# Kernel tuning notes

Hardware: AMD Instinct MI355X
Metric: run time of the kernel (lower is better)

## Reference

```python
import math
import jax, jax.numpy as jnp
import numpy as np

N_HEADS = 8

def setup_inputs() -> dict:
    key = jax.random.key(0)
    bs, n_heads, ch, l = 4, N_HEADS, 64, 1024
    width = 3 * n_heads * ch      # 1536 (packed q,k,v channels)
    T = 3 * l                     # 3072 (three spatial bands: ll, lh, hl)
    qkv = jax.random.normal(key, (bs, width, T), dtype=jnp.float32)
    return {"qkv": qkv, "l": l}

def reference(qkv, l):
    n_heads = N_HEADS
    bs, width, T = qkv.shape
    ch = width // (3 * n_heads)
    q, k, v = jnp.split(qkv, 3, axis=1)              # each (bs, n_heads*ch, T)
    scale = 1.0 / math.sqrt(math.sqrt(ch))
    qh = (q * scale).reshape(bs * n_heads, ch, T)
    kh = (k * scale).reshape(bs * n_heads, ch, T)
    vh = v.reshape(bs * n_heads, ch, T)
    # The original computes attention separately for q[:, :, :l], [l:2l], [2l:],
    # but k/v (and the softmax axis s) are identical, so computing attention
    # over the full query once and splitting the output is the same math.
    attn = jnp.einsum('bct,bcs->bts', qh, kh)        # (bs*H, T, T)
    w = jax.nn.softmax(attn.astype(jnp.float32), axis=-1).astype(attn.dtype)
    agg = jnp.einsum('bts,bcs->bct', w, vh).reshape(bs, n_heads * ch, T)
    return (agg[:, :, :l], agg[:, :, l:2 * l], agg[:, :, 2 * l:])
```

## Files before the change

### kernel.cpp

```cpp
#include <hip/hip_runtime.h>
#include <hip/hip_bf16.h>
#include <stdint.h>

#define T      3072
#define CH     64
#define HEADS  32
#define BM     128
#define BN     64
#define NIT    (T / BN)

typedef unsigned short u16;
typedef short short8 __attribute__((ext_vector_type(8)));
typedef float floatx4 __attribute__((ext_vector_type(4)));

__device__ __forceinline__ unsigned pk2(float a, float b) {
  union { __hip_bfloat162 h; unsigned u; } cv;
  cv.h = __float22bfloat162_rn(float2{a, b});
  return cv.u;
}

__device__ __forceinline__ void gl_lds16(const void* g, void* l) {
  __builtin_amdgcn_global_load_lds(
      (const __attribute__((address_space(1))) uint32_t*)g,
      (__attribute__((address_space(3))) uint32_t*)l, 16, 0, 0);
}

__device__ __forceinline__ void pl32swap(unsigned& x, unsigned& y) {
#if __has_builtin(__builtin_amdgcn_permlane32_swap)
  auto r = __builtin_amdgcn_permlane32_swap(x, y, false, false);
  x = r[0]; y = r[1];
#else
  asm("v_permlane32_swap_b32 %0, %1" : "+v"(x), "+v"(y));
#endif
}
__device__ __forceinline__ void pl16swap(unsigned& x, unsigned& y) {
#if __has_builtin(__builtin_amdgcn_permlane16_swap)
  auto r = __builtin_amdgcn_permlane16_swap(x, y, false, false);
  x = r[0]; y = r[1];
#else
  asm("v_permlane16_swap_b32 %0, %1" : "+v"(x), "+v"(y));
#endif
}

__global__ __launch_bounds__(256) void qktrans(
    const float* __restrict__ qkv, u16* __restrict__ Qt, u16* __restrict__ Kt,
    u16* __restrict__ Vo) {
  __shared__ __align__(16) u16 tl[64][72];
  const int ttile = blockIdx.x, hh = blockIdx.y, role = blockIdx.z;
  const int b = hh >> 3, h = hh & 7;
  const int t0 = ttile * 64;
  const int tid = threadIdx.x;

  if (role == 2) {
    const float* vsrc = qkv + (size_t)(b * 1536 + 1024 + h * CH) * T;
    u16* vdst = Vo + (size_t)(b * 512 + h * CH) * T;
#pragma unroll
    for (int p = 0; p < 2; ++p) {
      const int r = p * 32 + (tid >> 3);
      const int off = (tid & 7) * 8;
      const float4* s4 = (const float4*)(vsrc + (size_t)r * T + t0 + off);
      float4 a = s4[0], c = s4[1];
      uint4 o;
      o.x = pk2(a.x, a.y); o.y = pk2(a.z, a.w);
      o.z = pk2(c.x, c.y); o.w = pk2(c.z, c.w);
      *(uint4*)(vdst + (size_t)r * T + t0 + off) = o;
    }
    return;
  }

  const float* src = qkv + (size_t)(b * 1536 + role * 512 + h * CH) * T;
  const float scale = (role == 0) ? 0.18033688011112042f : 1.0f;

#pragma unroll
  for (int p = 0; p < 2; ++p) {
    const int c0 = p * 32 + ((tid >> 4) << 1);
    const int ts = (tid & 15) * 4;
    float4 a = *(const float4*)(src + (size_t)c0 * T + t0 + ts);
    float4 c = *(const float4*)(src + (size_t)(c0 + 1) * T + t0 + ts);
    *(unsigned*)&tl[ts + 0][c0] = pk2(a.x * scale, c.x * scale);
    *(unsigned*)&tl[ts + 1][c0] = pk2(a.y * scale, c.y * scale);
    *(unsigned*)&tl[ts + 2][c0] = pk2(a.z * scale, c.z * scale);
    *(unsigned*)&tl[ts + 3][c0] = pk2(a.w * scale, c.w * scale);
  }
  __syncthreads();
  u16* dst = (role == 0 ? Qt : Kt) + (size_t)hh * T * CH;
#pragma unroll
  for (int q = 0; q < 2; ++q) {
    const int t = q * 32 + (tid >> 3);
    const int cc = (tid & 7) * 8;
    uint4 v = *(const uint4*)&tl[t][cc];
    *(uint4*)(dst + (size_t)(t0 + t) * CH + cc) = v;
  }
}

__global__ __launch_bounds__(256, 3) void attn(
    const u16* __restrict__ Qt, const u16* __restrict__ Kt,
    const u16* __restrict__ Vg, float* __restrict__ out) {
  __shared__ __align__(16) u16 KB[2][BN * CH];
  __shared__ __align__(16) u16 VB[2][CH * BN];

  const int qtile = blockIdx.x, hh = blockIdx.y;
  const int tid = threadIdx.x;
  const int wave = tid >> 6, lane = tid & 63;
  const int l15 = lane & 15, quad = lane >> 4;
  const int t0 = qtile * BM + wave * 32;

  const u16* Qh = Qt + (size_t)hh * T * CH;
  const u16* Kh = Kt + (size_t)hh * T * CH;
  const u16* Vh = Vg + (size_t)hh * CH * T;

  short8 qf[2][2];
#pragma unroll
  for (int tq = 0; tq < 2; ++tq)
#pragma unroll
    for (int kc = 0; kc < 2; ++kc)
      qf[tq][kc] = *(const short8*)(Qh + (size_t)(t0 + tq * 16 + l15) * CH + kc * 32 + quad * 8);

  floatx4 oacc[2][4] = {};
  float lsum[2][2] = {};

  int srow[2], scb[2];
#pragma unroll
  for (int j = 0; j < 2; ++j) {
    const int p = wave * 128 + j * 64 + lane;
    srow[j] = p >> 3;
    scb[j]  = (p & 7) ^ ((srow[j] + 2 * (srow[j] >> 3)) & 7);
  }
  const int swl = (l15 + 2 * (l15 >> 3)) & 7;

#define STAGE(buf, s0)                                                              \
  do {                                                                              \
    _Pragma("unroll")                                                               \
    for (int j = 0; j < 2; ++j)                                                     \
      gl_lds16(Kh + (size_t)((s0) + srow[j]) * CH + scb[j] * 8,                     \
               &KB[buf][(wave * 128 + j * 64) * 8]);                                \
    _Pragma("unroll")                                                               \
    for (int j = 0; j < 2; ++j)                                                     \
      gl_lds16(Vh + (size_t)srow[j] * T + (s0) + scb[j] * 8,                        \
               &VB[buf][(wave * 128 + j * 64) * 8]);                                \
  } while (0)

  STAGE(0, 0);

  for (int it = 0; it < NIT; ++it) {
    const int cur = it & 1;
    __syncthreads();
    if (it + 1 < NIT) STAGE(cur ^ 1, (it + 1) * BN);

    const u16* KL = KB[cur];
    const u16* VL = VB[cur];

    floatx4 sacc[2][4];
#pragma unroll
    for (int nt = 0; nt < 4; ++nt) {
      const int ph0 = quad ^ swl ^ ((nt & 1) * 4);
      const int base = (nt * 16 + l15) * CH;
      const short8 kf0 = *(const short8*)(KL + base + ph0 * 8);
      const short8 kf1 = *(const short8*)(KL + base + (ph0 ^ 4) * 8);
#pragma unroll
      for (int tq = 0; tq < 2; ++tq) {
        floatx4 z = {0.f, 0.f, 0.f, 0.f};
        z = __builtin_amdgcn_mfma_f32_16x16x32_bf16(kf0, qf[tq][0], z, 0, 0, 0);
        z = __builtin_amdgcn_mfma_f32_16x16x32_bf16(kf1, qf[tq][1], z, 0, 0, 0);
        sacc[tq][nt] = z;
      }
    }

    unsigned Apk[2][4], Bpk[2][4];
#pragma unroll
    for (int tq = 0; tq < 2; ++tq)
#pragma unroll
      for (int nt = 0; nt < 4; ++nt) {
        floatx4 sv = sacc[tq][nt];
        float p0 = __builtin_amdgcn_exp2f(sv[0]);
        float p1 = __builtin_amdgcn_exp2f(sv[1]);
        float p2 = __builtin_amdgcn_exp2f(sv[2]);
        float p3 = __builtin_amdgcn_exp2f(sv[3]);
        lsum[tq][nt & 1] += (p0 + p1) + (p2 + p3);
        Apk[tq][nt] = pk2(p0, p1);
        Bpk[tq][nt] = pk2(p2, p3);
      }

#pragma unroll
    for (int ks = 0; ks < 2; ++ks) {
      short8 pf[2];
#pragma unroll
      for (int tq = 0; tq < 2; ++tq) {
        unsigned a0 = Apk[tq][2 * ks], a1 = Apk[tq][2 * ks + 1];
        unsigned b0 = Bpk[tq][2 * ks], b1 = Bpk[tq][2 * ks + 1];
        pl32swap(a0, a1); pl16swap(a0, a1);
        pl32swap(b0, b1); pl16swap(b0, b1);
        union { uint4 u; short8 s; } pw;
        pw.u.x = a0; pw.u.y = b0; pw.u.z = a1; pw.u.w = b1;
        pf[tq] = pw.s;
      }
#pragma unroll
      for (int mt = 0; mt < 4; ++mt) {
        const int ph = quad ^ swl ^ ((mt & 1) * 4) ^ (ks * 4);
        const short8 vf = *(const short8*)(VL + (mt * 16 + l15) * BN + ph * 8);
        oacc[0][mt] = __builtin_amdgcn_mfma_f32_16x16x32_bf16(pf[0], vf, oacc[0][mt], 0, 0, 0);
        oacc[1][mt] = __builtin_amdgcn_mfma_f32_16x16x32_bf16(pf[1], vf, oacc[1][mt], 0, 0, 0);
      }
    }
  }

  float ls[2];
#pragma unroll
  for (int tq = 0; tq < 2; ++tq) {
    float s = lsum[tq][0] + lsum[tq][1];
    s += __shfl_xor(s, 16, 64);
    s += __shfl_xor(s, 32, 64);
    ls[tq] = s;
  }
  float linv[2][4];
#pragma unroll
  for (int tq = 0; tq < 2; ++tq)
#pragma unroll
    for (int r = 0; r < 4; ++r)
      linv[tq][r] = 1.0f / __shfl(ls[tq], quad * 4 + r, 64);

  const int b = hh >> 3, h = hh & 7;
#pragma unroll
  for (int tq = 0; tq < 2; ++tq) {
    const int tg = t0 + tq * 16 + quad * 4;
    const int band = tg >> 10, tt = tg & 1023;
    float* obase = out + (size_t)band * (4 * 512 * 1024)
                       + (size_t)b * (512 * 1024)
                       + (size_t)(h * CH) * 1024 + tt;
#pragma unroll
    for (int mt = 0; mt < 4; ++mt) {
      const int c = mt * 16 + l15;
      float4 v;
      v.x = oacc[tq][mt][0] * linv[tq][0];
      v.y = oacc[tq][mt][1] * linv[tq][1];
      v.z = oacc[tq][mt][2] * linv[tq][2];
      v.w = oacc[tq][mt][3] * linv[tq][3];
      *(float4*)(obase + (size_t)c * 1024) = v;
    }
  }
}

extern "C" void kernel_launch(void* const* d_in, const int* in_sizes, int n_in,
                              void* d_out, int out_size, void* d_ws, size_t ws_size,
                              hipStream_t stream) {
  (void)in_sizes; (void)n_in; (void)out_size; (void)ws_size;
  const float* qkv = (const float*)d_in[0];
  u16* Qt = (u16*)d_ws;
  u16* Kt = Qt + (size_t)HEADS * T * CH;
  u16* Vo = Kt + (size_t)HEADS * T * CH;
  float* out = (float*)d_out;

  qktrans<<<dim3(T / 64, HEADS, 3), 256, 0, stream>>>(qkv, Qt, Kt, Vo);
  attn<<<dim3(T / BM, HEADS), 256, 0, stream>>>(Qt, Kt, Vo, out);
}
```

Baseline: 218.5 us.

## Split query tile across 8 waves and compute row sums via MFMA

The attention block now uses 512 threads (8 waves), each owning 16 query rows instead of 32. This halves per-wave register state and doubles wave-level parallelism. The per-row softmax denominator is now accumulated by an extra MFMA against a ones vector, replacing the VALU adds and cross-lane shuffles. In exchange, each K/V tile loaded into LDS is reused across fewer MFMAs per wave, and the rowsum is computed from bf16-rounded probabilities.

```diff
diff --git a/kernel.cpp b/kernel.cpp
--- a/kernel.cpp
+++ b/kernel.cpp
@@ -93,7 +93,7 @@
   }
 }
 
-__global__ __launch_bounds__(256, 3) void attn(
+__global__ __launch_bounds__(512, 6) void attn(
     const u16* __restrict__ Qt, const u16* __restrict__ Kt,
     const u16* __restrict__ Vg, float* __restrict__ out) {
   __shared__ __align__(16) u16 KB[2][BN * CH];
@@ -103,41 +103,33 @@
   const int tid = threadIdx.x;
   const int wave = tid >> 6, lane = tid & 63;
   const int l15 = lane & 15, quad = lane >> 4;
-  const int t0 = qtile * BM + wave * 32;
+  const int t0 = qtile * BM + wave * 16;
 
   const u16* Qh = Qt + (size_t)hh * T * CH;
   const u16* Kh = Kt + (size_t)hh * T * CH;
   const u16* Vh = Vg + (size_t)hh * CH * T;
 
-  short8 qf[2][2];
-#pragma unroll
-  for (int tq = 0; tq < 2; ++tq)
-#pragma unroll
-    for (int kc = 0; kc < 2; ++kc)
-      qf[tq][kc] = *(const short8*)(Qh + (size_t)(t0 + tq * 16 + l15) * CH + kc * 32 + quad * 8);
-
-  floatx4 oacc[2][4] = {};
-  float lsum[2][2] = {};
-
-  int srow[2], scb[2];
-#pragma unroll
-  for (int j = 0; j < 2; ++j) {
-    const int p = wave * 128 + j * 64 + lane;
-    srow[j] = p >> 3;
-    scb[j]  = (p & 7) ^ ((srow[j] + 2 * (srow[j] >> 3)) & 7);
-  }
+  short8 qf[2];
+#pragma unroll
+  for (int kc = 0; kc < 2; ++kc)
+    qf[kc] = *(const short8*)(Qh + (size_t)(t0 + l15) * CH + kc * 32 + quad * 8);
+
+  short8 ones = {0x3F80, 0x3F80, 0x3F80, 0x3F80, 0x3F80, 0x3F80, 0x3F80, 0x3F80};
+
+  floatx4 oacc[4] = {};
+  floatx4 lacc = {0.f, 0.f, 0.f, 0.f};
+
+  const int p = wave * 64 + lane;
+  const int srow = p >> 3;
+  const int scb = (p & 7) ^ ((srow + 2 * (srow >> 3)) & 7);
   const int swl = (l15 + 2 * (l15 >> 3)) & 7;
 
 #define STAGE(buf, s0)                                                              \
   do {                                                                              \
-    _Pragma("unroll")                                                               \
-    for (int j = 0; j < 2; ++j)                                                     \
-      gl_lds16(Kh + (size_t)((s0) + srow[j]) * CH + scb[j] * 8,                     \
-               &KB[buf][(wave * 128 + j * 64) * 8]);                                \
-    _Pragma("unroll")                                                               \
-    for (int j = 0; j < 2; ++j)                                                     \
-      gl_lds16(Vh + (size_t)srow[j] * T + (s0) + scb[j] * 8,                        \
-               &VB[buf][(wave * 128 + j * 64) * 8]);                                \
+    gl_lds16(Kh + (size_t)((s0) + srow) * CH + scb * 8,                             \
+             &KB[buf][(wave * 64) * 8]);                                            \
+    gl_lds16(Vh + (size_t)srow * T + (s0) + scb * 8,                                \
+             &VB[buf][(wave * 64) * 8]);                                            \
   } while (0)
 
   STAGE(0, 0);
@@ -150,93 +142,69 @@
     const u16* KL = KB[cur];
     const u16* VL = VB[cur];
 
-    floatx4 sacc[2][4];
+    floatx4 sacc[4];
 #pragma unroll
     for (int nt = 0; nt < 4; ++nt) {
       const int ph0 = quad ^ swl ^ ((nt & 1) * 4);
       const int base = (nt * 16 + l15) * CH;
       const short8 kf0 = *(const short8*)(KL + base + ph0 * 8);
       const short8 kf1 = *(const short8*)(KL + base + (ph0 ^ 4) * 8);
-#pragma unroll
-      for (int tq = 0; tq < 2; ++tq) {
-        floatx4 z = {0.f, 0.f, 0.f, 0.f};
-        z = __builtin_amdgcn_mfma_f32_16x16x32_bf16(kf0, qf[tq][0], z, 0, 0, 0);
-        z = __builtin_amdgcn_mfma_f32_16x16x32_bf16(kf1, qf[tq][1], z, 0, 0, 0);
-        sacc[tq][nt] = z;
-      }
-    }
-
-    unsigned Apk[2][4], Bpk[2][4];
-#pragma unroll
-    for (int tq = 0; tq < 2; ++tq)
-#pragma unroll
-      for (int nt = 0; nt < 4; ++nt) {
-        floatx4 sv = sacc[tq][nt];
-        float p0 = __builtin_amdgcn_exp2f(sv[0]);
-        float p1 = __builtin_amdgcn_exp2f(sv[1]);
-        float p2 = __builtin_amdgcn_exp2f(sv[2]);
-        float p3 = __builtin_amdgcn_exp2f(sv[3]);
-        lsum[tq][nt & 1] += (p0 + p1) + (p2 + p3);
-        Apk[tq][nt] = pk2(p0, p1);
-        Bpk[tq][nt] = pk2(p2, p3);
-      }
+      floatx4 z = {0.f, 0.f, 0.f, 0.f};
+      z = __builtin_amdgcn_mfma_f32_16x16x32_bf16(kf0, qf[0], z, 0, 0, 0);
+      z = __builtin_amdgcn_mfma_f32_16x16x32_bf16(kf1, qf[1], z, 0, 0, 0);
+      sacc[nt] = z;
+    }
+
+    unsigned Apk[4], Bpk[4];
+#pragma unroll
+    for (int nt = 0; nt < 4; ++nt) {
+      floatx4 sv = sacc[nt];
+      float p0 = __builtin_amdgcn_exp2f(sv[0]);
+      float p1 = __builtin_amdgcn_exp2f(sv[1]);
+      float p2 = __builtin_amdgcn_exp2f(sv[2]);
+      float p3 = __builtin_amdgcn_exp2f(sv[3]);
+      Apk[nt] = pk2(p0, p1);
+      Bpk[nt] = pk2(p2, p3);
+    }
 
 #pragma unroll
     for (int ks = 0; ks < 2; ++ks) {
-      short8 pf[2];
-#pragma unroll
-      for (int tq = 0; tq < 2; ++tq) {
-        unsigned a0 = Apk[tq][2 * ks], a1 = Apk[tq][2 * ks + 1];
-        unsigned b0 = Bpk[tq][2 * ks], b1 = Bpk[tq][2 * ks + 1];
-        pl32swap(a0, a1); pl16swap(a0, a1);
-        pl32swap(b0, b1); pl16swap(b0, b1);
-        union { uint4 u; short8 s; } pw;
-        pw.u.x = a0; pw.u.y = b0; pw.u.z = a1; pw.u.w = b1;
-        pf[tq] = pw.s;
-      }
+      unsigned a0 = Apk[2 * ks], a1 = Apk[2 * ks + 1];
+      unsigned b0 = Bpk[2 * ks], b1 = Bpk[2 * ks + 1];
+      pl32swap(a0, a1); pl16swap(a0, a1);
+      pl32swap(b0, b1); pl16swap(b0, b1);
+      union { uint4 u; short8 s; } pw;
+      pw.u.x = a0; pw.u.y = b0; pw.u.z = a1; pw.u.w = b1;
+      const short8 pf = pw.s;
+      lacc = __builtin_amdgcn_mfma_f32_16x16x32_bf16(pf, ones, lacc, 0, 0, 0);
 #pragma unroll
       for (int mt = 0; mt < 4; ++mt) {
         const int ph = quad ^ swl ^ ((mt & 1) * 4) ^ (ks * 4);
         const short8 vf = *(const short8*)(VL + (mt * 16 + l15) * BN + ph * 8);
-        oacc[0][mt] = __builtin_amdgcn_mfma_f32_16x16x32_bf16(pf[0], vf, oacc[0][mt], 0, 0, 0);
-        oacc[1][mt] = __builtin_amdgcn_mfma_f32_16x16x32_bf16(pf[1], vf, oacc[1][mt], 0, 0, 0);
+        oacc[mt] = __builtin_amdgcn_mfma_f32_16x16x32_bf16(pf, vf, oacc[mt], 0, 0, 0);
       }
     }
   }
 
-  float ls[2];
-#pragma unroll
-  for (int tq = 0; tq < 2; ++tq) {
-    float s = lsum[tq][0] + lsum[tq][1];
-    s += __shfl_xor(s, 16, 64);
-    s += __shfl_xor(s, 32, 64);
-    ls[tq] = s;
-  }
-  float linv[2][4];
-#pragma unroll
-  for (int tq = 0; tq < 2; ++tq)
-#pragma unroll
-    for (int r = 0; r < 4; ++r)
-      linv[tq][r] = 1.0f / __shfl(ls[tq], quad * 4 + r, 64);
+  float linv[4];
+#pragma unroll
+  for (int r = 0; r < 4; ++r) linv[r] = 1.0f / lacc[r];
 
   const int b = hh >> 3, h = hh & 7;
-#pragma unroll
-  for (int tq = 0; tq < 2; ++tq) {
-    const int tg = t0 + tq * 16 + quad * 4;
-    const int band = tg >> 10, tt = tg & 1023;
-    float* obase = out + (size_t)band * (4 * 512 * 1024)
-                       + (size_t)b * (512 * 1024)
-                       + (size_t)(h * CH) * 1024 + tt;
-#pragma unroll
-    for (int mt = 0; mt < 4; ++mt) {
-      const int c = mt * 16 + l15;
-      float4 v;
-      v.x = oacc[tq][mt][0] * linv[tq][0];
-      v.y = oacc[tq][mt][1] * linv[tq][1];
-      v.z = oacc[tq][mt][2] * linv[tq][2];
-      v.w = oacc[tq][mt][3] * linv[tq][3];
-      *(float4*)(obase + (size_t)c * 1024) = v;
-    }
+  const int tg = t0 + quad * 4;
+  const int band = tg >> 10, tt = tg & 1023;
+  float* obase = out + (size_t)band * (4 * 512 * 1024)
+                     + (size_t)b * (512 * 1024)
+                     + (size_t)(h * CH) * 1024 + tt;
+#pragma unroll
+  for (int mt = 0; mt < 4; ++mt) {
+    const int c = mt * 16 + l15;
+    float4 v;
+    v.x = oacc[mt][0] * linv[0];
+    v.y = oacc[mt][1] * linv[1];
+    v.z = oacc[mt][2] * linv[2];
+    v.w = oacc[mt][3] * linv[3];
+    *(float4*)(obase + (size_t)c * 1024) = v;
   }
 }
 
@@ -251,5 +219,5 @@
   float* out = (float*)d_out;
 
   qktrans<<<dim3(T / 64, HEADS, 3), 256, 0, stream>>>(qkv, Qt, Kt, Vo);
-  attn<<<dim3(T / BM, HEADS), 256, 0, stream>>>(Qt, Kt, Vo, out);
-}
+  attn<<<dim3(T / BM, HEADS), 512, 0, stream>>>(Qt, Kt, Vo, out);
+}
```

Result: no change. 214.3 us (-1.9%).

## Split KV range across two wave groups, fuse Q conversion into attention

Applied to the files above, without the earlier changes.

The attention kernel now runs 512 threads, with two wave groups that each process half of every pair of 64-key blocks. Their partial outputs and row sums are combined through LDS at the end. Q is read directly from the fp32 input, scaled and converted inside the attention kernel, so the prep pass now handles only K and V. Row sums are computed with an MFMA against a ones vector instead of scalar adds, and V staging is restructured with an extra barrier per iteration. The aim is more parallelism per tile and one less global round trip for Q, at the cost of more barriers, the cross-group reduction, and strided uncoalesced Q loads.

```diff
diff --git a/kernel.cpp b/kernel.cpp
--- a/kernel.cpp
+++ b/kernel.cpp
@@ -7,7 +7,7 @@
 #define HEADS  32
 #define BM     128
 #define BN     64
-#define NIT    (T / BN)
+#define NIT2   (T / (2 * BN))
 
 typedef unsigned short u16;
 typedef short short8 __attribute__((ext_vector_type(8)));
@@ -42,16 +42,14 @@
 #endif
 }
 
-__global__ __launch_bounds__(256) void qktrans(
-    const float* __restrict__ qkv, u16* __restrict__ Qt, u16* __restrict__ Kt,
-    u16* __restrict__ Vo) {
-  __shared__ __align__(16) u16 tl[64][72];
+__global__ __launch_bounds__(256) void prep(
+    const float* __restrict__ qkv, u16* __restrict__ Kt, u16* __restrict__ Vo) {
   const int ttile = blockIdx.x, hh = blockIdx.y, role = blockIdx.z;
   const int b = hh >> 3, h = hh & 7;
   const int t0 = ttile * 64;
   const int tid = threadIdx.x;
 
-  if (role == 2) {
+  if (role == 1) {
     const float* vsrc = qkv + (size_t)(b * 1536 + 1024 + h * CH) * T;
     u16* vdst = Vo + (size_t)(b * 512 + h * CH) * T;
 #pragma unroll
@@ -68,22 +66,22 @@
     return;
   }
 
-  const float* src = qkv + (size_t)(b * 1536 + role * 512 + h * CH) * T;
-  const float scale = (role == 0) ? 0.18033688011112042f : 1.0f;
-
+  __shared__ __align__(16) u16 tl[64][72];
+  const float* src = qkv + (size_t)(b * 1536 + 512 + h * CH) * T;
+  const int tb = tid & 15;
 #pragma unroll
   for (int p = 0; p < 2; ++p) {
     const int c0 = p * 32 + ((tid >> 4) << 1);
-    const int ts = (tid & 15) * 4;
-    float4 a = *(const float4*)(src + (size_t)c0 * T + t0 + ts);
-    float4 c = *(const float4*)(src + (size_t)(c0 + 1) * T + t0 + ts);
-    *(unsigned*)&tl[ts + 0][c0] = pk2(a.x * scale, c.x * scale);
-    *(unsigned*)&tl[ts + 1][c0] = pk2(a.y * scale, c.y * scale);
-    *(unsigned*)&tl[ts + 2][c0] = pk2(a.z * scale, c.z * scale);
-    *(unsigned*)&tl[ts + 3][c0] = pk2(a.w * scale, c.w * scale);
+    const float* r0 = src + (size_t)c0 * T + t0;
+    const float* r1 = r0 + T;
+#pragma unroll
+    for (int k = 0; k < 4; ++k) {
+      const int t = tb + 16 * k;
+      *(unsigned*)&tl[t][c0] = pk2(r0[t], r1[t]);
+    }
   }
   __syncthreads();
-  u16* dst = (role == 0 ? Qt : Kt) + (size_t)hh * T * CH;
+  u16* dst = Kt + (size_t)hh * T * CH;
 #pragma unroll
   for (int q = 0; q < 2; ++q) {
     const int t = q * 32 + (tid >> 3);
@@ -93,62 +91,81 @@
   }
 }
 
-__global__ __launch_bounds__(256, 3) void attn(
-    const u16* __restrict__ Qt, const u16* __restrict__ Kt,
+__global__ __launch_bounds__(512, 6) void attn(
+    const float* __restrict__ qkv, const u16* __restrict__ Kt,
     const u16* __restrict__ Vg, float* __restrict__ out) {
-  __shared__ __align__(16) u16 KB[2][BN * CH];
-  __shared__ __align__(16) u16 VB[2][CH * BN];
+  __shared__ __align__(16) u16 SMEM[24576];
+  u16* KBp = SMEM;
+  u16* VBp = SMEM + 16384;
 
   const int qtile = blockIdx.x, hh = blockIdx.y;
   const int tid = threadIdx.x;
   const int wave = tid >> 6, lane = tid & 63;
+  const int tg = wave & 3, sg = wave >> 2;
   const int l15 = lane & 15, quad = lane >> 4;
-  const int t0 = qtile * BM + wave * 32;
-
-  const u16* Qh = Qt + (size_t)hh * T * CH;
+  const int t0 = qtile * BM + tg * 32;
+  const int b = hh >> 3, h = hh & 7;
+
   const u16* Kh = Kt + (size_t)hh * T * CH;
   const u16* Vh = Vg + (size_t)hh * CH * T;
 
+  const float QS = 0.18033688011112042f;
+  const float* Qsrc = qkv + (size_t)(b * 1536 + h * CH) * T;
   short8 qf[2][2];
 #pragma unroll
   for (int tq = 0; tq < 2; ++tq)
 #pragma unroll
-    for (int kc = 0; kc < 2; ++kc)
-      qf[tq][kc] = *(const short8*)(Qh + (size_t)(t0 + tq * 16 + l15) * CH + kc * 32 + quad * 8);
+    for (int kc = 0; kc < 2; ++kc) {
+      const float* col = Qsrc + (size_t)(kc * 32 + quad * 8) * T + (t0 + tq * 16 + l15);
+      float f[8];
+#pragma unroll
+      for (int j = 0; j < 8; ++j) f[j] = col[(size_t)j * T] * QS;
+      union { uint4 u; short8 s; } q_;
+      q_.u.x = pk2(f[0], f[1]); q_.u.y = pk2(f[2], f[3]);
+      q_.u.z = pk2(f[4], f[5]); q_.u.w = pk2(f[6], f[7]);
+      qf[tq][kc] = q_.s;
+    }
+
+  const short8 ones = {0x3F80, 0x3F80, 0x3F80, 0x3F80, 0x3F80, 0x3F80, 0x3F80, 0x3F80};
 
   floatx4 oacc[2][4] = {};
-  float lsum[2][2] = {};
-
-  int srow[2], scb[2];
-#pragma unroll
-  for (int j = 0; j < 2; ++j) {
-    const int p = wave * 128 + j * 64 + lane;
-    srow[j] = p >> 3;
-    scb[j]  = (p & 7) ^ ((srow[j] + 2 * (srow[j] >> 3)) & 7);
-  }
+  floatx4 lacc[2] = {};
+
+  const int p = tid;
+  const int srow = p >> 3;
+  const int scb = (p & 7) ^ ((srow + 2 * (srow >> 3)) & 7);
   const int swl = (l15 + 2 * (l15 >> 3)) & 7;
 
-#define STAGE(buf, s0)                                                              \
+#define STAGE_K(buf, jt1)                                                           \
   do {                                                                              \
     _Pragma("unroll")                                                               \
-    for (int j = 0; j < 2; ++j)                                                     \
-      gl_lds16(Kh + (size_t)((s0) + srow[j]) * CH + scb[j] * 8,                     \
-               &KB[buf][(wave * 128 + j * 64) * 8]);                                \
+    for (int sgX = 0; sgX < 2; ++sgX) {                                             \
+      const int s0 = (2 * (jt1) + sgX) * BN;                                        \
+      gl_lds16(Kh + (size_t)(s0 + srow) * CH + scb * 8,                             \
+               KBp + ((buf) * 2 + sgX) * 4096 + wave * 512);                        \
+    }                                                                               \
+  } while (0)
+
+#define STAGE_V(jt)                                                                 \
+  do {                                                                              \
     _Pragma("unroll")                                                               \
-    for (int j = 0; j < 2; ++j)                                                     \
-      gl_lds16(Vh + (size_t)srow[j] * T + (s0) + scb[j] * 8,                        \
-               &VB[buf][(wave * 128 + j * 64) * 8]);                                \
+    for (int sgX = 0; sgX < 2; ++sgX) {                                             \
+      const int s0 = (2 * (jt) + sgX) * BN;                                         \
+      gl_lds16(Vh + (size_t)srow * T + s0 + scb * 8,                                \
+               VBp + sgX * 4096 + wave * 512);                                      \
+    }                                                                               \
   } while (0)
 
-  STAGE(0, 0);
-
-  for (int it = 0; it < NIT; ++it) {
-    const int cur = it & 1;
+  STAGE_K(0, 0);
+  int cur = 0;
+
+  for (int jt = 0; jt < NIT2; ++jt) {
     __syncthreads();
-    if (it + 1 < NIT) STAGE(cur ^ 1, (it + 1) * BN);
-
-    const u16* KL = KB[cur];
-    const u16* VL = VB[cur];
+    STAGE_V(jt);
+    if (jt + 1 < NIT2) STAGE_K(cur ^ 1, jt + 1);
+
+    const u16* KL = KBp + (cur * 2 + sg) * 4096;
+    const u16* VL = VBp + sg * 4096;
 
     floatx4 sacc[2][4];
 #pragma unroll
@@ -176,10 +193,11 @@
         float p1 = __builtin_amdgcn_exp2f(sv[1]);
         float p2 = __builtin_amdgcn_exp2f(sv[2]);
         float p3 = __builtin_amdgcn_exp2f(sv[3]);
-        lsum[tq][nt & 1] += (p0 + p1) + (p2 + p3);
         Apk[tq][nt] = pk2(p0, p1);
         Bpk[tq][nt] = pk2(p2, p3);
       }
+
+    __syncthreads();
 
 #pragma unroll
     for (int ks = 0; ks < 2; ++ks) {
@@ -193,6 +211,7 @@
         union { uint4 u; short8 s; } pw;
         pw.u.x = a0; pw.u.y = b0; pw.u.z = a1; pw.u.w = b1;
         pf[tq] = pw.s;
+        lacc[tq] = __builtin_amdgcn_mfma_f32_16x16x32_bf16(pf[tq], ones, lacc[tq], 0, 0, 0);
       }
 #pragma unroll
       for (int mt = 0; mt < 4; ++mt) {
@@ -202,40 +221,54 @@
         oacc[1][mt] = __builtin_amdgcn_mfma_f32_16x16x32_bf16(pf[1], vf, oacc[1][mt], 0, 0, 0);
       }
     }
-  }
-
-  float ls[2];
-#pragma unroll
-  for (int tq = 0; tq < 2; ++tq) {
-    float s = lsum[tq][0] + lsum[tq][1];
-    s += __shfl_xor(s, 16, 64);
-    s += __shfl_xor(s, 32, 64);
-    ls[tq] = s;
-  }
-  float linv[2][4];
-#pragma unroll
-  for (int tq = 0; tq < 2; ++tq)
-#pragma unroll
-    for (int r = 0; r < 4; ++r)
-      linv[tq][r] = 1.0f / __shfl(ls[tq], quad * 4 + r, 64);
-
-  const int b = hh >> 3, h = hh & 7;
-#pragma unroll
-  for (int tq = 0; tq < 2; ++tq) {
-    const int tg = t0 + tq * 16 + quad * 4;
-    const int band = tg >> 10, tt = tg & 1023;
-    float* obase = out + (size_t)band * (4 * 512 * 1024)
-                       + (size_t)b * (512 * 1024)
-                       + (size_t)(h * CH) * 1024 + tt;
-#pragma unroll
-    for (int mt = 0; mt < 4; ++mt) {
-      const int c = mt * 16 + l15;
-      float4 v;
-      v.x = oacc[tq][mt][0] * linv[tq][0];
-      v.y = oacc[tq][mt][1] * linv[tq][1];
-      v.z = oacc[tq][mt][2] * linv[tq][2];
-      v.w = oacc[tq][mt][3] * linv[tq][3];
-      *(float4*)(obase + (size_t)c * 1024) = v;
+    cur ^= 1;
+  }
+
+  __syncthreads();
+  float* CMB = (float*)SMEM;
+  float* reg = CMB + tg * 2560;
+  if (sg == 1) {
+#pragma unroll
+    for (int tq = 0; tq < 2; ++tq) {
+#pragma unroll
+      for (int mt = 0; mt < 4; ++mt)
+        *(floatx4*)(reg + ((tq * 4 + mt) * 64 + lane) * 4) = oacc[tq][mt];
+      *(floatx4*)(reg + 2048 + (tq * 64 + lane) * 4) = lacc[tq];
+    }
+  }
+  __syncthreads();
+  if (sg == 0) {
+#pragma unroll
+    for (int tq = 0; tq < 2; ++tq) {
+#pragma unroll
+      for (int mt = 0; mt < 4; ++mt)
+        oacc[tq][mt] += *(const floatx4*)(reg + ((tq * 4 + mt) * 64 + lane) * 4);
+      lacc[tq] += *(const floatx4*)(reg + 2048 + (tq * 64 + lane) * 4);
+    }
+
+    float linv[2][4];
+#pragma unroll
+    for (int tq = 0; tq < 2; ++tq)
+#pragma unroll
+      for (int r = 0; r < 4; ++r) linv[tq][r] = 1.0f / lacc[tq][r];
+
+#pragma unroll
+    for (int tq = 0; tq < 2; ++tq) {
+      const int tgr = t0 + tq * 16 + quad * 4;
+      const int band = tgr >> 10, tt = tgr & 1023;
+      float* obase = out + (size_t)band * (4 * 512 * 1024)
+                         + (size_t)b * (512 * 1024)
+                         + (size_t)(h * CH) * 1024 + tt;
+#pragma unroll
+      for (int mt = 0; mt < 4; ++mt) {
+        const int c = mt * 16 + l15;
+        float4 v;
+        v.x = oacc[tq][mt][0] * linv[tq][0];
+        v.y = oacc[tq][mt][1] * linv[tq][1];
+        v.z = oacc[tq][mt][2] * linv[tq][2];
+        v.w = oacc[tq][mt][3] * linv[tq][3];
+        *(float4*)(obase + (size_t)c * 1024) = v;
+      }
     }
   }
 }
@@ -245,11 +278,10 @@
                               hipStream_t stream) {
   (void)in_sizes; (void)n_in; (void)out_size; (void)ws_size;
   const float* qkv = (const float*)d_in[0];
-  u16* Qt = (u16*)d_ws;
-  u16* Kt = Qt + (size_t)HEADS * T * CH;
+  u16* Kt = (u16*)d_ws;
   u16* Vo = Kt + (size_t)HEADS * T * CH;
   float* out = (float*)d_out;
 
-  qktrans<<<dim3(T / 64, HEADS, 3), 256, 0, stream>>>(qkv, Qt, Kt, Vo);
-  attn<<<dim3(T / BM, HEADS), 256, 0, stream>>>(Qt, Kt, Vo, out);
-}
+  prep<<<dim3(T / 64, HEADS, 2), 256, 0, stream>>>(qkv, Kt, Vo);
+  attn<<<dim3(T / BM, HEADS), 512, 0, stream>>>(qkv, Kt, Vo, out);
+}
```

Result: slower. 445.9 us (+104.1%).

## Use 6-wave 192-row query tiles, split K/V staging roles, MFMA row sums

Applied to the files above, without the earlier changes.

Raises the query tile from 128 to 192 rows with six waves per block, so each staged K/V tile is reused across more queries and the grid shrinks to 16x32 blocks. K and V loading is split by wave role: four waves load K and two load V. The softmax row sum now comes from an extra MFMA against a ones vector instead of scalar adds and shuffles. s_setprio brackets the MFMA phases to favour matrix issue. The trade-offs are fewer blocks in the grid, an extra MFMA per k-step, and uneven load work across waves.

```diff
diff --git a/kernel.cpp b/kernel.cpp
--- a/kernel.cpp
+++ b/kernel.cpp
@@ -5,7 +5,7 @@
 #define T      3072
 #define CH     64
 #define HEADS  32
-#define BM     128
+#define BM     192
 #define BN     64
 #define NIT    (T / BN)
 
@@ -93,7 +93,7 @@
   }
 }
 
-__global__ __launch_bounds__(256, 3) void attn(
+__global__ __launch_bounds__(384, 4) void attn(
     const u16* __restrict__ Qt, const u16* __restrict__ Kt,
     const u16* __restrict__ Vg, float* __restrict__ out) {
   __shared__ __align__(16) u16 KB[2][BN * CH];
@@ -104,6 +104,7 @@
   const int wave = tid >> 6, lane = tid & 63;
   const int l15 = lane & 15, quad = lane >> 4;
   const int t0 = qtile * BM + wave * 32;
+  const int b = hh >> 3, h = hh & 7;
 
   const u16* Qh = Qt + (size_t)hh * T * CH;
   const u16* Kh = Kt + (size_t)hh * T * CH;
@@ -116,28 +117,38 @@
     for (int kc = 0; kc < 2; ++kc)
       qf[tq][kc] = *(const short8*)(Qh + (size_t)(t0 + tq * 16 + l15) * CH + kc * 32 + quad * 8);
 
+  const short8 ones = {0x3F80, 0x3F80, 0x3F80, 0x3F80, 0x3F80, 0x3F80, 0x3F80, 0x3F80};
+
   floatx4 oacc[2][4] = {};
-  float lsum[2][2] = {};
-
-  int srow[2], scb[2];
-#pragma unroll
-  for (int j = 0; j < 2; ++j) {
-    const int p = wave * 128 + j * 64 + lane;
-    srow[j] = p >> 3;
-    scb[j]  = (p & 7) ^ ((srow[j] + 2 * (srow[j] >> 3)) & 7);
-  }
+  floatx4 lacc[2] = {};
+
+  const bool krole = (wave < 4);
+  const int lslot = krole ? wave * 64 + lane : (wave - 4) * 64 + lane;
+  const int step = krole ? 256 : 128;
+  int sr[4], sc[4];
+#pragma unroll
+  for (int j = 0; j < 4; ++j) {
+    const int p = (lslot + j * step) & 511;
+    sr[j] = p >> 3;
+    sc[j] = (p & 7) ^ ((sr[j] + 2 * (sr[j] >> 3)) & 7);
+  }
+  const int wb_k = wave * 64;
+  const int wb_v = (wave - 4) * 64;
   const int swl = (l15 + 2 * (l15 >> 3)) & 7;
 
 #define STAGE(buf, s0)                                                              \
   do {                                                                              \
-    _Pragma("unroll")                                                               \
-    for (int j = 0; j < 2; ++j)                                                     \
-      gl_lds16(Kh + (size_t)((s0) + srow[j]) * CH + scb[j] * 8,                     \
-               &KB[buf][(wave * 128 + j * 64) * 8]);                                \
-    _Pragma("unroll")                                                               \
-    for (int j = 0; j < 2; ++j)                                                     \
-      gl_lds16(Vh + (size_t)srow[j] * T + (s0) + scb[j] * 8,                        \
-               &VB[buf][(wave * 128 + j * 64) * 8]);                                \
+    if (krole) {                                                                    \
+      _Pragma("unroll")                                                             \
+      for (int j = 0; j < 2; ++j)                                                   \
+        gl_lds16(Kh + (size_t)((s0) + sr[j]) * CH + sc[j] * 8,                      \
+                 &KB[buf][(wb_k + j * 256) * 8]);                                   \
+    } else {                                                                        \
+      _Pragma("unroll")                                                             \
+      for (int j = 0; j < 4; ++j)                                                   \
+        gl_lds16(Vh + (size_t)sr[j] * T + (s0) + sc[j] * 8,                         \
+                 &VB[buf][(wb_v + j * 128) * 8]);                                   \
+    }                                                                               \
   } while (0)
 
   STAGE(0, 0);
@@ -151,6 +162,7 @@
     const u16* VL = VB[cur];
 
     floatx4 sacc[2][4];
+    __builtin_amdgcn_s_setprio(1);
 #pragma unroll
     for (int nt = 0; nt < 4; ++nt) {
       const int ph0 = quad ^ swl ^ ((nt & 1) * 4);
@@ -165,6 +177,7 @@
         sacc[tq][nt] = z;
       }
     }
+    __builtin_amdgcn_s_setprio(0);
 
     unsigned Apk[2][4], Bpk[2][4];
 #pragma unroll
@@ -176,11 +189,11 @@
         float p1 = __builtin_amdgcn_exp2f(sv[1]);
         float p2 = __builtin_amdgcn_exp2f(sv[2]);
         float p3 = __builtin_amdgcn_exp2f(sv[3]);
-        lsum[tq][nt & 1] += (p0 + p1) + (p2 + p3);
         Apk[tq][nt] = pk2(p0, p1);
         Bpk[tq][nt] = pk2(p2, p3);
       }
 
+    __builtin_amdgcn_s_setprio(1);
 #pragma unroll
     for (int ks = 0; ks < 2; ++ks) {
       short8 pf[2];
@@ -193,6 +206,7 @@
         union { uint4 u; short8 s; } pw;
         pw.u.x = a0; pw.u.y = b0; pw.u.z = a1; pw.u.w = b1;
         pf[tq] = pw.s;
+        lacc[tq] = __builtin_amdgcn_mfma_f32_16x16x32_bf16(pf[tq], ones, lacc[tq], 0, 0, 0);
       }
 #pragma unroll
       for (int mt = 0; mt < 4; ++mt) {
@@ -202,28 +216,19 @@
         oacc[1][mt] = __builtin_amdgcn_mfma_f32_16x16x32_bf16(pf[1], vf, oacc[1][mt], 0, 0, 0);
       }
     }
-  }
-
-  float ls[2];
+    __builtin_amdgcn_s_setprio(0);
+  }
+
+  float linv[2][4];
+#pragma unroll
+  for (int tq = 0; tq < 2; ++tq)
+#pragma unroll
+    for (int r = 0; r < 4; ++r) linv[tq][r] = 1.0f / lacc[tq][r];
+
 #pragma unroll
   for (int tq = 0; tq < 2; ++tq) {
-    float s = lsum[tq][0] + lsum[tq][1];
-    s += __shfl_xor(s, 16, 64);
-    s += __shfl_xor(s, 32, 64);
-    ls[tq] = s;
-  }
-  float linv[2][4];
-#pragma unroll
-  for (int tq = 0; tq < 2; ++tq)
-#pragma unroll
-    for (int r = 0; r < 4; ++r)
-      linv[tq][r] = 1.0f / __shfl(ls[tq], quad * 4 + r, 64);
-
-  const int b = hh >> 3, h = hh & 7;
-#pragma unroll
-  for (int tq = 0; tq < 2; ++tq) {
-    const int tg = t0 + tq * 16 + quad * 4;
-    const int band = tg >> 10, tt = tg & 1023;
+    const int tgr = t0 + tq * 16 + quad * 4;
+    const int band = tgr >> 10, tt = tgr & 1023;
     float* obase = out + (size_t)band * (4 * 512 * 1024)
                        + (size_t)b * (512 * 1024)
                        + (size_t)(h * CH) * 1024 + tt;
@@ -251,5 +256,5 @@
   float* out = (float*)d_out;
 
   qktrans<<<dim3(T / 64, HEADS, 3), 256, 0, stream>>>(qkv, Qt, Kt, Vo);
-  attn<<<dim3(T / BM, HEADS), 256, 0, stream>>>(Qt, Kt, Vo, out);
-}
+  attn<<<dim3(T / BM, HEADS), 384, 0, stream>>>(Qt, Kt, Vo, out);
+}
```

New measurement: 222.6 us. No clear change (+1.9%).
